# Performance work log

Hardware: AMD Instinct MI355X
Metric: run time of the kernel (lower is better)

The kernel has to match this reference:

```python
import jax, jax.numpy as jnp
import numpy as np

N_NODES = 50000
N_EDGES = 1600000
NODE_DIM = 64
EDGE_DIM = 64
HID = 64
EPS = 1e-5


def _linear(x, W, b):
    return x @ W + b


def _layernorm(x, g, b):
    m = jnp.mean(x, axis=-1, keepdims=True)
    v = jnp.mean((x - m) ** 2, axis=-1, keepdims=True)
    return (x - m) * jax.lax.rsqrt(v + EPS) * g + b


def _mlp(x, p, pre):
    # Linear-ReLU, Linear-ReLU, Linear-LayerNorm
    h = jax.nn.relu(_linear(x, p[pre + 'W1'], p[pre + 'b1']))
    h = jax.nn.relu(_linear(h, p[pre + 'W2'], p[pre + 'b2']))
    h = _linear(h, p[pre + 'W3'], p[pre + 'b3'])
    return _layernorm(h, p[pre + 'g'], p[pre + 'beta'])


def setup_inputs() -> dict:
    key = jax.random.key(0)
    ks = jax.random.split(key, 16)
    inp = {
        'node_feat': jax.random.normal(ks[0], (N_NODES, NODE_DIM), jnp.float32),
        'edge_feat': jax.random.normal(ks[1], (N_EDGES, EDGE_DIM), jnp.float32),
        'edge_idx': jax.random.randint(ks[2], (N_EDGES, 2), 0, N_NODES, jnp.int32),
        'node_size': N_NODES,
    }
    s = 0.05
    e_in = EDGE_DIM + 2 * NODE_DIM
    n_in = NODE_DIM + EDGE_DIM
    inp['eW1'] = jax.random.normal(ks[3], (e_in, HID), jnp.float32) * s
    inp['eb1'] = jnp.zeros((HID,), jnp.float32)
    inp['eW2'] = jax.random.normal(ks[4], (HID, HID), jnp.float32) * s
    inp['eb2'] = jnp.zeros((HID,), jnp.float32)
    inp['eW3'] = jax.random.normal(ks[5], (HID, HID), jnp.float32) * s
    inp['eb3'] = jnp.zeros((HID,), jnp.float32)
    inp['eg'] = jnp.ones((HID,), jnp.float32)
    inp['ebeta'] = jnp.zeros((HID,), jnp.float32)
    inp['nW1'] = jax.random.normal(ks[6], (n_in, HID), jnp.float32) * s
    inp['nb1'] = jnp.zeros((HID,), jnp.float32)
    inp['nW2'] = jax.random.normal(ks[7], (HID, HID), jnp.float32) * s
    inp['nb2'] = jnp.zeros((HID,), jnp.float32)
    inp['nW3'] = jax.random.normal(ks[8], (HID, HID), jnp.float32) * s
    inp['nb3'] = jnp.zeros((HID,), jnp.float32)
    inp['ng'] = jnp.ones((HID,), jnp.float32)
    inp['nbeta'] = jnp.zeros((HID,), jnp.float32)
    return inp


def reference(node_feat, edge_feat, edge_idx, node_size,
              eW1, eb1, eW2, eb2, eW3, eb3, eg, ebeta,
              nW1, nb1, nW2, nb2, nW3, nb3, ng, nbeta):
    p = dict(eW1=eW1, eb1=eb1, eW2=eW2, eb2=eb2, eW3=eW3, eb3=eb3, eg=eg, ebeta=ebeta,
             nW1=nW1, nb1=nb1, nW2=nW2, nb2=nb2, nW3=nW3, nb3=nb3, ng=ng, nbeta=nbeta)
    center = edge_idx[:, 0]
    source = edge_idx[:, 1]
    # [E, edge_dim + 2*node_dim]
    stacked = jnp.concatenate([edge_feat, node_feat[center], node_feat[source]], axis=1)
    proc_edge_feat = _mlp(stacked, p, 'e')  # [E, 64]
    # scatter-add aggregate to nodes
    nodal_edge_feat = jax.ops.segment_sum(proc_edge_feat, center, num_segments=node_size)
    stacked_node = jnp.concatenate([node_feat, nodal_edge_feat], axis=1)  # [N, node_dim+64]
    proc_node_feat = _mlp(stacked_node, p, 'n')  # [N, 64]
    return proc_edge_feat, proc_node_feat
```

## Files before the change

kernel.cpp:

```cpp
#include <hip/hip_runtime.h>

typedef unsigned short u16;
typedef unsigned int u32;
typedef __attribute__((ext_vector_type(8))) __bf16 bf16x8;
typedef __attribute__((ext_vector_type(4))) float f32x4;
typedef __attribute__((ext_vector_type(2))) u32 u32x2;
typedef __attribute__((ext_vector_type(4))) u32 u32x4;

__device__ __forceinline__ u16 f2bf(float f) {
    u32 u = __float_as_uint(f);
    u = (u + 0x7FFFu + ((u >> 16) & 1u)) >> 16;
    return (u16)u;
}
__device__ __forceinline__ bf16x8 cvt2bf(f32x4 lo, f32x4 hi) {
    bf16x8 r;
    r[0] = (__bf16)lo[0]; r[1] = (__bf16)lo[1]; r[2] = (__bf16)lo[2]; r[3] = (__bf16)lo[3];
    r[4] = (__bf16)hi[0]; r[5] = (__bf16)hi[1]; r[6] = (__bf16)hi[2]; r[7] = (__bf16)hi[3];
    return r;
}
__device__ __forceinline__ bf16x8 load8f_bf(const float* p) {
    return cvt2bf(*(const f32x4*)p, *(const f32x4*)(p + 4));
}
__device__ __forceinline__ u32 pk2(float x, float y) {
    __bf16 bx = (__bf16)x, by = (__bf16)y;
    return (u32)__builtin_bit_cast(u16, bx) | ((u32)__builtin_bit_cast(u16, by) << 16);
}

#define PK_EW1 0
#define PK_EW2 12288
#define PK_EW3 16384
#define PK_NW1 20480
#define PK_NW2 28672
#define PK_NW3 32768
#define PK_TOTAL 36864

__global__ void pack_weights_kernel(const float* __restrict__ eW1, const float* __restrict__ eW2,
                                    const float* __restrict__ eW3, const float* __restrict__ nW1,
                                    const float* __restrict__ nW2, const float* __restrict__ nW3,
                                    u16* __restrict__ P) {
    int idx = blockIdx.x * blockDim.x + threadIdx.x;
    if (idx >= PK_TOTAL) return;
    const float* W; int base;
    if (idx < PK_EW2)      { W = eW1; base = PK_EW1; }
    else if (idx < PK_EW3) { W = eW2; base = PK_EW2; }
    else if (idx < PK_NW1) { W = eW3; base = PK_EW3; }
    else if (idx < PK_NW2) { W = nW1; base = PK_NW1; }
    else if (idx < PK_NW3) { W = nW2; base = PK_NW2; }
    else                   { W = nW3; base = PK_NW3; }
    int r = idx - base;
    int j = r & 7, lane = (r >> 3) & 63, m = (r >> 9) & 3, s = r >> 11;
    int k = s * 32 + (lane >> 4) * 8 + j;
    int col = 16 * m + (lane & 15);
    P[idx] = f2bf(W[k * 64 + col]);
}

__global__ void degree_kernel(const int* __restrict__ edge_idx, int* __restrict__ deg, int E) {
    int e = blockIdx.x * blockDim.x + threadIdx.x;
    if (e < E) atomicAdd(&deg[edge_idx[2 * e]], 1);
}

__global__ void scan_blocks_kernel(const int* __restrict__ deg, int* __restrict__ off,
                                   int* __restrict__ partials, int N) {
    __shared__ int sh[256];
    const int t = threadIdx.x;
    const int g = blockIdx.x * 256 + t;
    int v = (g < N) ? deg[g] : 0;
    sh[t] = v;
    __syncthreads();
#pragma unroll
    for (int d = 1; d < 256; d <<= 1) {
        int add = (t >= d) ? sh[t - d] : 0;
        __syncthreads();
        sh[t] += add;
        __syncthreads();
    }
    if (g < N) off[g] = sh[t] - v;
    if (t == 255) partials[blockIdx.x] = sh[255];
}

__global__ void scan_partials_kernel(int* __restrict__ partials, int nparts) {
    __shared__ int sh[256];
    const int t = threadIdx.x;
    int v = (t < nparts) ? partials[t] : 0;
    sh[t] = v;
    __syncthreads();
#pragma unroll
    for (int d = 1; d < 256; d <<= 1) {
        int add = (t >= d) ? sh[t - d] : 0;
        __syncthreads();
        sh[t] += add;
        __syncthreads();
    }
    if (t < nparts) partials[t] = sh[t] - v;
}

__global__ void finalize_offsets_kernel(int* __restrict__ off, int* __restrict__ pos,
                                        const int* __restrict__ partials, int N, int E) {
    int g = blockIdx.x * blockDim.x + threadIdx.x;
    if (g < N) {
        int o = off[g] + partials[g >> 8];
        off[g] = o;
        pos[g] = o;
    }
    if (g == 0) off[N] = E;
}

__global__ void fill_csr_kernel(const int* __restrict__ edge_idx, int* __restrict__ pos,
                                int* __restrict__ csr, int E) {
    int e = blockIdx.x * blockDim.x + threadIdx.x;
    if (e < E) {
        int slot = atomicAdd(&pos[edge_idx[2 * e]], 1);
        csr[slot] = e;
    }
}

__global__ __launch_bounds__(256) void gather_kernel(
    const float* __restrict__ proc_edge, const int* __restrict__ off,
    const int* __restrict__ csr, u16* __restrict__ nodal16, int N)
{
    const int wid = threadIdx.x >> 6, lane = threadIdx.x & 63;
    const int n = blockIdx.x * 4 + wid;
    if (n >= N) return;
    const int r = lane >> 4;
    const int q = lane & 15;
    const int beg = off[n], end = off[n + 1];
    f32x4 v0 = 0.0f, v1 = 0.0f, v2 = 0.0f, v3 = 0.0f;
    int j = beg + r;
    for (; j + 12 < end; j += 16) {
        int e0 = csr[j], e1 = csr[j + 4], e2 = csr[j + 8], e3 = csr[j + 12];
        v0 += *(const f32x4*)(proc_edge + (size_t)e0 * 64 + q * 4);
        v1 += *(const f32x4*)(proc_edge + (size_t)e1 * 64 + q * 4);
        v2 += *(const f32x4*)(proc_edge + (size_t)e2 * 64 + q * 4);
        v3 += *(const f32x4*)(proc_edge + (size_t)e3 * 64 + q * 4);
    }
    for (; j < end; j += 4) {
        int e0 = csr[j];
        v0 += *(const f32x4*)(proc_edge + (size_t)e0 * 64 + q * 4);
    }
    v0 += v1; v2 += v3; v0 += v2;
#pragma unroll
    for (int i = 0; i < 4; ++i) {
        v0[i] += __shfl_xor(v0[i], 16, 64);
        v0[i] += __shfl_xor(v0[i], 32, 64);
    }
    if (r == 0) {
        u32x2 pv; pv[0] = pk2(v0[0], v0[1]); pv[1] = pk2(v0[2], v0[3]);
        *(u32x2*)(nodal16 + (size_t)n * 64 + q * 4) = pv;
    }
}

#define ET 2
__global__ __launch_bounds__(512, 6) void edge_mlp_kernel(
    const float* __restrict__ node_feat, const float* __restrict__ edge_feat,
    const int* __restrict__ edge_idx, const u16* __restrict__ Pw,
    const float* __restrict__ b1g, const float* __restrict__ b2g, const float* __restrict__ b3g,
    const float* __restrict__ gg, const float* __restrict__ betag,
    float* __restrict__ out_edge, int E)
{
    __shared__ u16 wlds[12288];
    __shared__ u16 htile[8][1024];
    __shared__ float params[5][64];
    const int tid = threadIdx.x;
#pragma unroll
    for (int i = 0; i < 3; ++i) {
        int idx = i * 512 + tid;
        *(u32x4*)(wlds + (size_t)idx * 8) = *(const u32x4*)(Pw + PK_EW1 + (size_t)idx * 8);
    }
    if (tid < 64) {
        params[0][tid] = b1g[tid];
        params[1][tid] = b2g[tid];
        params[2][tid] = b3g[tid];
        params[3][tid] = gg[tid];
        params[4][tid] = betag[tid];
    }
    __syncthreads();

    const int wid = tid >> 6, lane = tid & 63;
    const int er = lane & 15, a = lane >> 4;
    const int ebase = (blockIdx.x * 8 + wid) * (16 * ET);
    u16* ht = htile[wid];
    const int swz = (er & 7) << 4;

    int eidx[ET], cn[ET], sn[ET];
#pragma unroll
    for (int t = 0; t < ET; ++t) {
        int e = ebase + t * 16 + er;
        if (e > E - 1) e = E - 1;
        eidx[t] = e;
        int2 ii = *(const int2*)(edge_idx + 2 * e);
        cn[t] = ii.x; sn[t] = ii.y;
    }

    f32x4 acc[ET][4];
#pragma unroll
    for (int t = 0; t < ET; ++t)
#pragma unroll
        for (int m = 0; m < 4; ++m) acc[t][m] = 0.0f;

#pragma unroll
    for (int t = 0; t < ET; ++t) {
        f32x4 raw[12];
#pragma unroll
        for (int s = 0; s < 6; ++s) {
            const float* src;
            if (s < 2)      src = edge_feat + (size_t)eidx[t] * 64 + s * 32 + a * 8;
            else if (s < 4) src = node_feat + (size_t)cn[t] * 64 + (s - 2) * 32 + a * 8;
            else            src = node_feat + (size_t)sn[t] * 64 + (s - 4) * 32 + a * 8;
            raw[2 * s]     = *(const f32x4*)src;
            raw[2 * s + 1] = *(const f32x4*)(src + 4);
        }
#pragma unroll
        for (int s = 0; s < 6; ++s) {
            bf16x8 bf = cvt2bf(raw[2 * s], raw[2 * s + 1]);
#pragma unroll
            for (int m = 0; m < 4; ++m) {
                bf16x8 af = *(const bf16x8*)(wlds + ((s * 4 + m) * 64 + lane) * 8);
                acc[t][m] = __builtin_amdgcn_mfma_f32_16x16x32_bf16(af, bf, acc[t][m], 0, 0, 0);
            }
        }
    }
    __syncthreads();
#pragma unroll
    for (int i = 0; i < 2; ++i) {
        int idx = i * 512 + tid;
        *(u32x4*)(wlds + (size_t)idx * 8) = *(const u32x4*)(Pw + PK_EW2 + (size_t)idx * 8);
    }
    __syncthreads();

#pragma unroll
    for (int t = 0; t < ET; ++t) {
#pragma unroll
        for (int m = 0; m < 4; ++m) {
            float v0 = fmaxf(acc[t][m][0] + params[0][16 * m + 4 * a + 0], 0.0f);
            float v1 = fmaxf(acc[t][m][1] + params[0][16 * m + 4 * a + 1], 0.0f);
            float v2 = fmaxf(acc[t][m][2] + params[0][16 * m + 4 * a + 2], 0.0f);
            float v3 = fmaxf(acc[t][m][3] + params[0][16 * m + 4 * a + 3], 0.0f);
            u32x2 pv; pv[0] = pk2(v0, v1); pv[1] = pk2(v2, v3);
            int boff = (er * 128 + (16 * m + 4 * a) * 2) ^ swz;
            *(u32x2*)((char*)ht + boff) = pv;
        }
        f32x4 a2[4];
#pragma unroll
        for (int m = 0; m < 4; ++m) a2[m] = 0.0f;
#pragma unroll
        for (int s = 0; s < 2; ++s) {
            int boff = (er * 128 + s * 64 + a * 16) ^ swz;
            bf16x8 bf = *(const bf16x8*)((char*)ht + boff);
#pragma unroll
            for (int m = 0; m < 4; ++m) {
                bf16x8 af = *(const bf16x8*)(wlds + ((s * 4 + m) * 64 + lane) * 8);
                a2[m] = __builtin_amdgcn_mfma_f32_16x16x32_bf16(af, bf, a2[m], 0, 0, 0);
            }
        }
#pragma unroll
        for (int m = 0; m < 4; ++m) {
            float v0 = fmaxf(a2[m][0] + params[1][16 * m + 4 * a + 0], 0.0f);
            float v1 = fmaxf(a2[m][1] + params[1][16 * m + 4 * a + 1], 0.0f);
            float v2 = fmaxf(a2[m][2] + params[1][16 * m + 4 * a + 2], 0.0f);
            float v3 = fmaxf(a2[m][3] + params[1][16 * m + 4 * a + 3], 0.0f);
            u32x2 pv; pv[0] = pk2(v0, v1); pv[1] = pk2(v2, v3);
            int boff = (er * 128 + (16 * m + 4 * a) * 2) ^ swz;
            *(u32x2*)((char*)ht + boff) = pv;
        }
        f32x4 a3[4];
#pragma unroll
        for (int m = 0; m < 4; ++m) a3[m] = 0.0f;
#pragma unroll
        for (int s = 0; s < 2; ++s) {
            int boff = (er * 128 + s * 64 + a * 16) ^ swz;
            bf16x8 bf = *(const bf16x8*)((char*)ht + boff);
#pragma unroll
            for (int m = 0; m < 4; ++m) {
                bf16x8 af = *(const bf16x8*)(wlds + 4096 + ((s * 4 + m) * 64 + lane) * 8);
                a3[m] = __builtin_amdgcn_mfma_f32_16x16x32_bf16(af, bf, a3[m], 0, 0, 0);
            }
        }
        float vals[16], sum = 0.0f, ssq = 0.0f;
#pragma unroll
        for (int m = 0; m < 4; ++m)
#pragma unroll
            for (int r = 0; r < 4; ++r) {
                float v = a3[m][r] + params[2][16 * m + 4 * a + r];
                vals[4 * m + r] = v; sum += v; ssq += v * v;
            }
        sum += __shfl_xor(sum, 16, 64); sum += __shfl_xor(sum, 32, 64);
        ssq += __shfl_xor(ssq, 16, 64); ssq += __shfl_xor(ssq, 32, 64);
        const float mean = sum * 0.015625f;
        const float var = ssq * 0.015625f - mean * mean;
        const float inv = rsqrtf(var + 1e-5f);
        const int e = ebase + t * 16 + er;
        if (e < E) {
#pragma unroll
            for (int m = 0; m < 4; ++m) {
                f32x4 o;
#pragma unroll
                for (int r = 0; r < 4; ++r) {
                    int f = 16 * m + 4 * a + r;
                    o[r] = (vals[4 * m + r] - mean) * inv * params[3][f] + params[4][f];
                }
                *(f32x4*)(out_edge + (size_t)e * 64 + 16 * m + 4 * a) = o;
            }
        }
    }
}

__global__ __launch_bounds__(256) void node_mlp_kernel(
    const float* __restrict__ node_feat, const u16* __restrict__ nodal16,
    const u16* __restrict__ Pw,
    const float* __restrict__ b1g, const float* __restrict__ b2g, const float* __restrict__ b3g,
    const float* __restrict__ gg, const float* __restrict__ betag,
    float* __restrict__ out_node, int N)
{
    __shared__ float params[5][64];
    __shared__ u16 htile[4][1024];
    const int tid = threadIdx.x;
    if (tid < 64) {
        params[0][tid] = b1g[tid];
        params[1][tid] = b2g[tid];
        params[2][tid] = b3g[tid];
        params[3][tid] = gg[tid];
        params[4][tid] = betag[tid];
    }
    __syncthreads();
    const int wid = tid >> 6, lane = tid & 63;
    const int er = lane & 15, a = lane >> 4;
    const int nbase = (blockIdx.x * 4 + wid) * 16;
    if (nbase >= N) return;
    const int n = nbase + er;
    u16* ht = htile[wid];
    const int swz = (er & 7) << 4;

    f32x4 acc[4];
#pragma unroll
    for (int m = 0; m < 4; ++m) acc[m] = 0.0f;

#pragma unroll
    for (int s = 0; s < 4; ++s) {
        bf16x8 af[4];
#pragma unroll
        for (int m = 0; m < 4; ++m)
            af[m] = *(const bf16x8*)(Pw + PK_NW1 + ((s * 4 + m) * 64 + lane) * 8);
        bf16x8 bf;
        if (s < 2) bf = load8f_bf(node_feat + (size_t)n * 64 + s * 32 + a * 8);
        else       bf = *(const bf16x8*)(nodal16 + (size_t)n * 64 + (s - 2) * 32 + a * 8);
#pragma unroll
        for (int m = 0; m < 4; ++m)
            acc[m] = __builtin_amdgcn_mfma_f32_16x16x32_bf16(af[m], bf, acc[m], 0, 0, 0);
    }
#pragma unroll
    for (int m = 0; m < 4; ++m) {
        float v0 = fmaxf(acc[m][0] + params[0][16 * m + 4 * a + 0], 0.0f);
        float v1 = fmaxf(acc[m][1] + params[0][16 * m + 4 * a + 1], 0.0f);
        float v2 = fmaxf(acc[m][2] + params[0][16 * m + 4 * a + 2], 0.0f);
        float v3 = fmaxf(acc[m][3] + params[0][16 * m + 4 * a + 3], 0.0f);
        u32x2 pv; pv[0] = pk2(v0, v1); pv[1] = pk2(v2, v3);
        int boff = (er * 128 + (16 * m + 4 * a) * 2) ^ swz;
        *(u32x2*)((char*)ht + boff) = pv;
    }

#pragma unroll
    for (int m = 0; m < 4; ++m) acc[m] = 0.0f;
#pragma unroll
    for (int s = 0; s < 2; ++s) {
        bf16x8 af[4];
#pragma unroll
        for (int m = 0; m < 4; ++m)
            af[m] = *(const bf16x8*)(Pw + PK_NW2 + ((s * 4 + m) * 64 + lane) * 8);
        int boff = (er * 128 + s * 64 + a * 16) ^ swz;
        bf16x8 bf = *(const bf16x8*)((char*)ht + boff);
#pragma unroll
        for (int m = 0; m < 4; ++m)
            acc[m] = __builtin_amdgcn_mfma_f32_16x16x32_bf16(af[m], bf, acc[m], 0, 0, 0);
    }
#pragma unroll
    for (int m = 0; m < 4; ++m) {
        float v0 = fmaxf(acc[m][0] + params[1][16 * m + 4 * a + 0], 0.0f);
        float v1 = fmaxf(acc[m][1] + params[1][16 * m + 4 * a + 1], 0.0f);
        float v2 = fmaxf(acc[m][2] + params[1][16 * m + 4 * a + 2], 0.0f);
        float v3 = fmaxf(acc[m][3] + params[1][16 * m + 4 * a + 3], 0.0f);
        u32x2 pv; pv[0] = pk2(v0, v1); pv[1] = pk2(v2, v3);
        int boff = (er * 128 + (16 * m + 4 * a) * 2) ^ swz;
        *(u32x2*)((char*)ht + boff) = pv;
    }

#pragma unroll
    for (int m = 0; m < 4; ++m) acc[m] = 0.0f;
#pragma unroll
    for (int s = 0; s < 2; ++s) {
        bf16x8 af[4];
#pragma unroll
        for (int m = 0; m < 4; ++m)
            af[m] = *(const bf16x8*)(Pw + PK_NW3 + ((s * 4 + m) * 64 + lane) * 8);
        int boff = (er * 128 + s * 64 + a * 16) ^ swz;
        bf16x8 bf = *(const bf16x8*)((char*)ht + boff);
#pragma unroll
        for (int m = 0; m < 4; ++m)
            acc[m] = __builtin_amdgcn_mfma_f32_16x16x32_bf16(af[m], bf, acc[m], 0, 0, 0);
    }
    float vals[16], sum = 0.0f, ssq = 0.0f;
#pragma unroll
    for (int m = 0; m < 4; ++m)
#pragma unroll
        for (int r = 0; r < 4; ++r) {
            float v = acc[m][r] + params[2][16 * m + 4 * a + r];
            vals[4 * m + r] = v; sum += v; ssq += v * v;
        }
    sum += __shfl_xor(sum, 16, 64); sum += __shfl_xor(sum, 32, 64);
    ssq += __shfl_xor(ssq, 16, 64); ssq += __shfl_xor(ssq, 32, 64);
    const float mean = sum * 0.015625f;
    const float var = ssq * 0.015625f - mean * mean;
    const float inv = rsqrtf(var + 1e-5f);
#pragma unroll
    for (int m = 0; m < 4; ++m) {
        f32x4 o;
#pragma unroll
        for (int r = 0; r < 4; ++r) {
            int f = 16 * m + 4 * a + r;
            o[r] = (vals[4 * m + r] - mean) * inv * params[3][f] + params[4][f];
        }
        *(f32x4*)(out_node + (size_t)n * 64 + 16 * m + 4 * a) = o;
    }
}

extern "C" void kernel_launch(void* const* d_in, const int* in_sizes, int n_in,
                              void* d_out, int out_size, void* d_ws, size_t ws_size,
                              hipStream_t stream) {
    const float* node_feat = (const float*)d_in[0];
    const float* edge_feat = (const float*)d_in[1];
    const int* edge_idx  = (const int*)d_in[2];
    const float* eW1 = (const float*)d_in[4];
    const float* eb1 = (const float*)d_in[5];
    const float* eW2 = (const float*)d_in[6];
    const float* eb2 = (const float*)d_in[7];
    const float* eW3 = (const float*)d_in[8];
    const float* eb3 = (const float*)d_in[9];
    const float* eg  = (const float*)d_in[10];
    const float* ebt = (const float*)d_in[11];
    const float* nW1 = (const float*)d_in[12];
    const float* nb1 = (const float*)d_in[13];
    const float* nW2 = (const float*)d_in[14];
    const float* nb2 = (const float*)d_in[15];
    const float* nW3 = (const float*)d_in[16];
    const float* nb3 = (const float*)d_in[17];
    const float* ng  = (const float*)d_in[18];
    const float* nbt = (const float*)d_in[19];

    const int N = in_sizes[0] / 64;
    const int E = in_sizes[1] / 64;
    const int nparts = (N + 255) / 256;

    char* w = (char*)d_ws;
    int* off      = (int*)w;                    w += (size_t)(N + 1) * 4;
    int* pos      = (int*)w;                    w += (size_t)N * 4;
    int* partials = (int*)w;                    w += 256 * 4;
    int* csr      = (int*)w;                    w += (size_t)E * 4;
    u16* Pw       = (u16*)w;                    w += (size_t)PK_TOTAL * 2;
    u16* nodal16  = (u16*)w;

    float* out_edge = (float*)d_out;
    float* out_node = out_edge + (size_t)E * 64;

    pack_weights_kernel<<<(PK_TOTAL + 255) / 256, 256, 0, stream>>>(eW1, eW2, eW3, nW1, nW2, nW3, Pw);

    const int eblocks = (E + 255) / 256;
    edge_mlp_kernel<<<eblocks, 512, 0, stream>>>(node_feat, edge_feat, edge_idx, Pw,
                                                 eb1, eb2, eb3, eg, ebt, out_edge, E);

    hipMemsetAsync(pos, 0, (size_t)N * 4, stream);
    degree_kernel<<<(E + 255) / 256, 256, 0, stream>>>(edge_idx, pos, E);
    scan_blocks_kernel<<<nparts, 256, 0, stream>>>(pos, off, partials, N);
    scan_partials_kernel<<<1, 256, 0, stream>>>(partials, nparts);
    finalize_offsets_kernel<<<(N + 255) / 256, 256, 0, stream>>>(off, pos, partials, N, E);
    fill_csr_kernel<<<(E + 255) / 256, 256, 0, stream>>>(edge_idx, pos, csr, E);

    gather_kernel<<<(N + 3) / 4, 256, 0, stream>>>(out_edge, off, csr, nodal16, N);

    const int nblocks = (N + 63) / 64;
    node_mlp_kernel<<<nblocks, 256, 0, stream>>>(node_feat, nodal16, Pw,
                                                 nb1, nb2, nb3, ng, nbt, out_node, N);
}
```

Before: 570.6 us.

## Fuse segment-sum into edge MLP via CSR-ordered edges and atomic adds

Builds the CSR ordering before the edge MLP and processes edges in center-sorted order, so each wave's 16-edge tile shares center nodes. After layernorm, each wave writes its outputs to LDS, reduces runs of equal center indices, and atomically adds the partial sums into an fp32 nodal buffer. This removes the separate gather kernel and its re-read of the full edge output. In exchange, the edge kernel now gathers edge_feat and node_feat in scattered order, writes out_edge with scattered stores, uses fp32 atomics, and sums bf16-rounded values rather than fp32.

```diff
diff --git a/kernel.cpp b/kernel.cpp
--- a/kernel.cpp
+++ b/kernel.cpp
@@ -11,6 +11,9 @@
     u32 u = __float_as_uint(f);
     u = (u + 0x7FFFu + ((u >> 16) & 1u)) >> 16;
     return (u16)u;
+}
+__device__ __forceinline__ float bf2f(u16 h) {
+    return __uint_as_float(((u32)h) << 16);
 }
 __device__ __forceinline__ bf16x8 cvt2bf(f32x4 lo, f32x4 hi) {
     bf16x8 r;
@@ -114,51 +117,18 @@
     }
 }
 
-__global__ __launch_bounds__(256) void gather_kernel(
-    const float* __restrict__ proc_edge, const int* __restrict__ off,
-    const int* __restrict__ csr, u16* __restrict__ nodal16, int N)
-{
-    const int wid = threadIdx.x >> 6, lane = threadIdx.x & 63;
-    const int n = blockIdx.x * 4 + wid;
-    if (n >= N) return;
-    const int r = lane >> 4;
-    const int q = lane & 15;
-    const int beg = off[n], end = off[n + 1];
-    f32x4 v0 = 0.0f, v1 = 0.0f, v2 = 0.0f, v3 = 0.0f;
-    int j = beg + r;
-    for (; j + 12 < end; j += 16) {
-        int e0 = csr[j], e1 = csr[j + 4], e2 = csr[j + 8], e3 = csr[j + 12];
-        v0 += *(const f32x4*)(proc_edge + (size_t)e0 * 64 + q * 4);
-        v1 += *(const f32x4*)(proc_edge + (size_t)e1 * 64 + q * 4);
-        v2 += *(const f32x4*)(proc_edge + (size_t)e2 * 64 + q * 4);
-        v3 += *(const f32x4*)(proc_edge + (size_t)e3 * 64 + q * 4);
-    }
-    for (; j < end; j += 4) {
-        int e0 = csr[j];
-        v0 += *(const f32x4*)(proc_edge + (size_t)e0 * 64 + q * 4);
-    }
-    v0 += v1; v2 += v3; v0 += v2;
-#pragma unroll
-    for (int i = 0; i < 4; ++i) {
-        v0[i] += __shfl_xor(v0[i], 16, 64);
-        v0[i] += __shfl_xor(v0[i], 32, 64);
-    }
-    if (r == 0) {
-        u32x2 pv; pv[0] = pk2(v0[0], v0[1]); pv[1] = pk2(v0[2], v0[3]);
-        *(u32x2*)(nodal16 + (size_t)n * 64 + q * 4) = pv;
-    }
-}
-
 #define ET 2
 __global__ __launch_bounds__(512, 6) void edge_mlp_kernel(
     const float* __restrict__ node_feat, const float* __restrict__ edge_feat,
-    const int* __restrict__ edge_idx, const u16* __restrict__ Pw,
+    const int* __restrict__ edge_idx, const int* __restrict__ csr,
+    const u16* __restrict__ Pw,
     const float* __restrict__ b1g, const float* __restrict__ b2g, const float* __restrict__ b3g,
     const float* __restrict__ gg, const float* __restrict__ betag,
-    float* __restrict__ out_edge, int E)
+    float* __restrict__ out_edge, float* __restrict__ nodal, int E)
 {
     __shared__ u16 wlds[12288];
     __shared__ u16 htile[8][1024];
+    __shared__ int cnt[8][16];
     __shared__ float params[5][64];
     const int tid = threadIdx.x;
 #pragma unroll
@@ -177,15 +147,16 @@
 
     const int wid = tid >> 6, lane = tid & 63;
     const int er = lane & 15, a = lane >> 4;
-    const int ebase = (blockIdx.x * 8 + wid) * (16 * ET);
+    const int sbase = (blockIdx.x * 8 + wid) * (16 * ET);
     u16* ht = htile[wid];
     const int swz = (er & 7) << 4;
 
     int eidx[ET], cn[ET], sn[ET];
 #pragma unroll
     for (int t = 0; t < ET; ++t) {
-        int e = ebase + t * 16 + er;
-        if (e > E - 1) e = E - 1;
+        int slot = sbase + t * 16 + er;
+        if (slot > E - 1) slot = E - 1;
+        int e = csr[slot];
         eidx[t] = e;
         int2 ii = *(const int2*)(edge_idx + 2 * e);
         cn[t] = ii.x; sn[t] = ii.y;
@@ -288,24 +259,44 @@
         const float mean = sum * 0.015625f;
         const float var = ssq * 0.015625f - mean * mean;
         const float inv = rsqrtf(var + 1e-5f);
-        const int e = ebase + t * 16 + er;
-        if (e < E) {
-#pragma unroll
-            for (int m = 0; m < 4; ++m) {
-                f32x4 o;
-#pragma unroll
-                for (int r = 0; r < 4; ++r) {
-                    int f = 16 * m + 4 * a + r;
-                    o[r] = (vals[4 * m + r] - mean) * inv * params[3][f] + params[4][f];
+        const int slot = sbase + t * 16 + er;
+        const int e = eidx[t];
+#pragma unroll
+        for (int m = 0; m < 4; ++m) {
+            f32x4 o;
+#pragma unroll
+            for (int r = 0; r < 4; ++r) {
+                int f = 16 * m + 4 * a + r;
+                o[r] = (vals[4 * m + r] - mean) * inv * params[3][f] + params[4][f];
+            }
+            if (slot < E)
+                *(f32x4*)(out_edge + (size_t)e * 64 + 16 * m + 4 * a) = o;
+            u32x2 pv; pv[0] = pk2(o[0], o[1]); pv[1] = pk2(o[2], o[3]);
+            int boff = (er * 128 + (16 * m + 4 * a) * 2) ^ swz;
+            *(u32x2*)((char*)ht + boff) = pv;
+        }
+        if (a == 0) cnt[wid][er] = (slot < E) ? cn[t] : -1;
+        {
+            const int f = lane;
+            float accv = 0.0f;
+            int cprev = cnt[wid][0];
+#pragma unroll
+            for (int er2 = 0; er2 < 16; ++er2) {
+                int c = cnt[wid][er2];
+                if (c != cprev) {
+                    if (cprev >= 0) unsafeAtomicAdd(nodal + (size_t)cprev * 64 + f, accv);
+                    accv = 0.0f; cprev = c;
                 }
-                *(f32x4*)(out_edge + (size_t)e * 64 + 16 * m + 4 * a) = o;
-            }
+                int boff = (er2 * 128 + f * 2) ^ ((er2 & 7) << 4);
+                accv += bf2f(*(const u16*)((char*)ht + boff));
+            }
+            if (cprev >= 0) unsafeAtomicAdd(nodal + (size_t)cprev * 64 + f, accv);
         }
     }
 }
 
 __global__ __launch_bounds__(256) void node_mlp_kernel(
-    const float* __restrict__ node_feat, const u16* __restrict__ nodal16,
+    const float* __restrict__ node_feat, const float* __restrict__ nodal,
     const u16* __restrict__ Pw,
     const float* __restrict__ b1g, const float* __restrict__ b2g, const float* __restrict__ b3g,
     const float* __restrict__ gg, const float* __restrict__ betag,
@@ -342,7 +333,7 @@
             af[m] = *(const bf16x8*)(Pw + PK_NW1 + ((s * 4 + m) * 64 + lane) * 8);
         bf16x8 bf;
         if (s < 2) bf = load8f_bf(node_feat + (size_t)n * 64 + s * 32 + a * 8);
-        else       bf = *(const bf16x8*)(nodal16 + (size_t)n * 64 + (s - 2) * 32 + a * 8);
+        else       bf = load8f_bf(nodal + (size_t)n * 64 + (s - 2) * 32 + a * 8);
 #pragma unroll
         for (int m = 0; m < 4; ++m)
             acc[m] = __builtin_amdgcn_mfma_f32_16x16x32_bf16(af[m], bf, acc[m], 0, 0, 0);
@@ -455,27 +446,27 @@
     int* partials = (int*)w;                    w += 256 * 4;
     int* csr      = (int*)w;                    w += (size_t)E * 4;
     u16* Pw       = (u16*)w;                    w += (size_t)PK_TOTAL * 2;
-    u16* nodal16  = (u16*)w;
+    w = (char*)(((size_t)w + 255) & ~(size_t)255);
+    float* nodal  = (float*)w;
 
     float* out_edge = (float*)d_out;
     float* out_node = out_edge + (size_t)E * 64;
 
     pack_weights_kernel<<<(PK_TOTAL + 255) / 256, 256, 0, stream>>>(eW1, eW2, eW3, nW1, nW2, nW3, Pw);
 
-    const int eblocks = (E + 255) / 256;
-    edge_mlp_kernel<<<eblocks, 512, 0, stream>>>(node_feat, edge_feat, edge_idx, Pw,
-                                                 eb1, eb2, eb3, eg, ebt, out_edge, E);
-
     hipMemsetAsync(pos, 0, (size_t)N * 4, stream);
+    hipMemsetAsync(nodal, 0, (size_t)N * 64 * 4, stream);
     degree_kernel<<<(E + 255) / 256, 256, 0, stream>>>(edge_idx, pos, E);
     scan_blocks_kernel<<<nparts, 256, 0, stream>>>(pos, off, partials, N);
     scan_partials_kernel<<<1, 256, 0, stream>>>(partials, nparts);
     finalize_offsets_kernel<<<(N + 255) / 256, 256, 0, stream>>>(off, pos, partials, N, E);
     fill_csr_kernel<<<(E + 255) / 256, 256, 0, stream>>>(edge_idx, pos, csr, E);
 
-    gather_kernel<<<(N + 3) / 4, 256, 0, stream>>>(out_edge, off, csr, nodal16, N);
+    const int eblocks = (E + 255) / 256;
+    edge_mlp_kernel<<<eblocks, 512, 0, stream>>>(node_feat, edge_feat, edge_idx, csr, Pw,
+                                                 eb1, eb2, eb3, eg, ebt, out_edge, nodal, E);
 
     const int nblocks = (N + 63) / 64;
-    node_mlp_kernel<<<nblocks, 256, 0, stream>>>(node_feat, nodal16, Pw,
+    node_mlp_kernel<<<nblocks, 256, 0, stream>>>(node_feat, nodal, Pw,
                                                  nb1, nb2, nb3, ng, nbt, out_node, N);
 }
```

New measurement: 558.7 us. 2.1% less time.

## Scatter edge outputs as bf16 into CSR-sorted buffer for contiguous segment gather

Applied to the files above, without the earlier changes.

The CSR build now runs before the edge MLP and records each edge's slot (rank). The edge MLP writes a bf16 copy of its output at that slot, so the node aggregation reads contiguous rows instead of random fp32 rows through the csr index. The edge kernel also keeps all three edge weight matrices resident in LDS, which removes the mid-kernel reload and its syncs, and it issues all raw loads before the MFMAs. In exchange it adds an extra 128 B per edge of scattered writes, lowers the occupancy hint from 6 to 4 blocks, and needs a large workspace, falling back to the old gather if the workspace is too small.

```diff
diff --git a/kernel.cpp b/kernel.cpp
--- a/kernel.cpp
+++ b/kernel.cpp
@@ -33,6 +33,7 @@
 #define PK_NW2 28672
 #define PK_NW3 32768
 #define PK_TOTAL 36864
+#define EW_U16 20480
 
 __global__ void pack_weights_kernel(const float* __restrict__ eW1, const float* __restrict__ eW2,
                                     const float* __restrict__ eW3, const float* __restrict__ nW1,
@@ -106,15 +107,56 @@
 }
 
 __global__ void fill_csr_kernel(const int* __restrict__ edge_idx, int* __restrict__ pos,
-                                int* __restrict__ csr, int E) {
+                                int* __restrict__ csr, int* __restrict__ rank, int E) {
     int e = blockIdx.x * blockDim.x + threadIdx.x;
     if (e < E) {
         int slot = atomicAdd(&pos[edge_idx[2 * e]], 1);
         csr[slot] = e;
-    }
-}
-
-__global__ __launch_bounds__(256) void gather_kernel(
+        rank[e] = slot;
+    }
+}
+
+__global__ __launch_bounds__(256) void gather_sorted_kernel(
+    const u16* __restrict__ sorted16, const int* __restrict__ off,
+    u16* __restrict__ nodal16, int N)
+{
+    const int wid = threadIdx.x >> 6, lane = threadIdx.x & 63;
+    const int n = blockIdx.x * 4 + wid;
+    if (n >= N) return;
+    const int g = lane >> 3;
+    const int c = lane & 7;
+    const int beg = off[n], end = off[n + 1];
+    float va[8], vb[8];
+#pragma unroll
+    for (int i = 0; i < 8; ++i) { va[i] = 0.0f; vb[i] = 0.0f; }
+    int j = beg + g;
+    for (; j + 8 < end; j += 16) {
+        bf16x8 v1 = *(const bf16x8*)(sorted16 + (size_t)j * 64 + c * 8);
+        bf16x8 v2 = *(const bf16x8*)(sorted16 + (size_t)(j + 8) * 64 + c * 8);
+#pragma unroll
+        for (int i = 0; i < 8; ++i) { va[i] += (float)v1[i]; vb[i] += (float)v2[i]; }
+    }
+    if (j < end) {
+        bf16x8 v1 = *(const bf16x8*)(sorted16 + (size_t)j * 64 + c * 8);
+#pragma unroll
+        for (int i = 0; i < 8; ++i) va[i] += (float)v1[i];
+    }
+#pragma unroll
+    for (int i = 0; i < 8; ++i) {
+        va[i] += vb[i];
+        va[i] += __shfl_xor(va[i], 8, 64);
+        va[i] += __shfl_xor(va[i], 16, 64);
+        va[i] += __shfl_xor(va[i], 32, 64);
+    }
+    if (g == 0) {
+        u32x4 q;
+        q[0] = pk2(va[0], va[1]); q[1] = pk2(va[2], va[3]);
+        q[2] = pk2(va[4], va[5]); q[3] = pk2(va[6], va[7]);
+        *(u32x4*)(nodal16 + (size_t)n * 64 + c * 8) = q;
+    }
+}
+
+__global__ __launch_bounds__(256) void gather_csr_kernel(
     const float* __restrict__ proc_edge, const int* __restrict__ off,
     const int* __restrict__ csr, u16* __restrict__ nodal16, int N)
 {
@@ -150,21 +192,22 @@
 }
 
 #define ET 2
-__global__ __launch_bounds__(512, 6) void edge_mlp_kernel(
+__global__ __launch_bounds__(512, 4) void edge_mlp_kernel(
     const float* __restrict__ node_feat, const float* __restrict__ edge_feat,
-    const int* __restrict__ edge_idx, const u16* __restrict__ Pw,
+    const int* __restrict__ edge_idx, const int* __restrict__ rank,
+    const u16* __restrict__ Pw,
     const float* __restrict__ b1g, const float* __restrict__ b2g, const float* __restrict__ b3g,
     const float* __restrict__ gg, const float* __restrict__ betag,
-    float* __restrict__ out_edge, int E)
+    float* __restrict__ out_edge, u16* __restrict__ sorted16, int E)
 {
-    __shared__ u16 wlds[12288];
+    __shared__ u16 wlds[EW_U16];
     __shared__ u16 htile[8][1024];
     __shared__ float params[5][64];
     const int tid = threadIdx.x;
 #pragma unroll
-    for (int i = 0; i < 3; ++i) {
+    for (int i = 0; i < 5; ++i) {
         int idx = i * 512 + tid;
-        *(u32x4*)(wlds + (size_t)idx * 8) = *(const u32x4*)(Pw + PK_EW1 + (size_t)idx * 8);
+        *(u32x4*)(wlds + (size_t)idx * 8) = *(const u32x4*)(Pw + (size_t)idx * 8);
     }
     if (tid < 64) {
         params[0][tid] = b1g[tid];
@@ -181,7 +224,7 @@
     u16* ht = htile[wid];
     const int swz = (er & 7) << 4;
 
-    int eidx[ET], cn[ET], sn[ET];
+    int eidx[ET], cn[ET], sn[ET], rk[ET];
 #pragma unroll
     for (int t = 0; t < ET; ++t) {
         int e = ebase + t * 16 + er;
@@ -189,43 +232,38 @@
         eidx[t] = e;
         int2 ii = *(const int2*)(edge_idx + 2 * e);
         cn[t] = ii.x; sn[t] = ii.y;
-    }
-
-    f32x4 acc[ET][4];
+        rk[t] = sorted16 ? rank[e] : 0;
+    }
+
+    f32x4 raw[ET][12];
 #pragma unroll
     for (int t = 0; t < ET; ++t)
-#pragma unroll
-        for (int m = 0; m < 4; ++m) acc[t][m] = 0.0f;
-
-#pragma unroll
-    for (int t = 0; t < ET; ++t) {
-        f32x4 raw[12];
 #pragma unroll
         for (int s = 0; s < 6; ++s) {
             const float* src;
             if (s < 2)      src = edge_feat + (size_t)eidx[t] * 64 + s * 32 + a * 8;
             else if (s < 4) src = node_feat + (size_t)cn[t] * 64 + (s - 2) * 32 + a * 8;
             else            src = node_feat + (size_t)sn[t] * 64 + (s - 4) * 32 + a * 8;
-            raw[2 * s]     = *(const f32x4*)src;
-            raw[2 * s + 1] = *(const f32x4*)(src + 4);
-        }
+            raw[t][2 * s]     = *(const f32x4*)src;
+            raw[t][2 * s + 1] = *(const f32x4*)(src + 4);
+        }
+
+    f32x4 acc[ET][4];
+#pragma unroll
+    for (int t = 0; t < ET; ++t)
+#pragma unroll
+        for (int m = 0; m < 4; ++m) acc[t][m] = 0.0f;
+#pragma unroll
+    for (int t = 0; t < ET; ++t)
 #pragma unroll
         for (int s = 0; s < 6; ++s) {
-            bf16x8 bf = cvt2bf(raw[2 * s], raw[2 * s + 1]);
+            bf16x8 bf = cvt2bf(raw[t][2 * s], raw[t][2 * s + 1]);
 #pragma unroll
             for (int m = 0; m < 4; ++m) {
-                bf16x8 af = *(const bf16x8*)(wlds + ((s * 4 + m) * 64 + lane) * 8);
+                bf16x8 af = *(const bf16x8*)(wlds + PK_EW1 + ((s * 4 + m) * 64 + lane) * 8);
                 acc[t][m] = __builtin_amdgcn_mfma_f32_16x16x32_bf16(af, bf, acc[t][m], 0, 0, 0);
             }
         }
-    }
-    __syncthreads();
-#pragma unroll
-    for (int i = 0; i < 2; ++i) {
-        int idx = i * 512 + tid;
-        *(u32x4*)(wlds + (size_t)idx * 8) = *(const u32x4*)(Pw + PK_EW2 + (size_t)idx * 8);
-    }
-    __syncthreads();
 
 #pragma unroll
     for (int t = 0; t < ET; ++t) {
@@ -248,7 +286,7 @@
             bf16x8 bf = *(const bf16x8*)((char*)ht + boff);
 #pragma unroll
             for (int m = 0; m < 4; ++m) {
-                bf16x8 af = *(const bf16x8*)(wlds + ((s * 4 + m) * 64 + lane) * 8);
+                bf16x8 af = *(const bf16x8*)(wlds + PK_EW2 + ((s * 4 + m) * 64 + lane) * 8);
                 a2[m] = __builtin_amdgcn_mfma_f32_16x16x32_bf16(af, bf, a2[m], 0, 0, 0);
             }
         }
@@ -271,7 +309,7 @@
             bf16x8 bf = *(const bf16x8*)((char*)ht + boff);
 #pragma unroll
             for (int m = 0; m < 4; ++m) {
-                bf16x8 af = *(const bf16x8*)(wlds + 4096 + ((s * 4 + m) * 64 + lane) * 8);
+                bf16x8 af = *(const bf16x8*)(wlds + PK_EW3 + ((s * 4 + m) * 64 + lane) * 8);
                 a3[m] = __builtin_amdgcn_mfma_f32_16x16x32_bf16(af, bf, a3[m], 0, 0, 0);
             }
         }
@@ -289,16 +327,20 @@
         const float var = ssq * 0.015625f - mean * mean;
         const float inv = rsqrtf(var + 1e-5f);
         const int e = ebase + t * 16 + er;
-        if (e < E) {
-#pragma unroll
-            for (int m = 0; m < 4; ++m) {
-                f32x4 o;
-#pragma unroll
-                for (int r = 0; r < 4; ++r) {
-                    int f = 16 * m + 4 * a + r;
-                    o[r] = (vals[4 * m + r] - mean) * inv * params[3][f] + params[4][f];
+#pragma unroll
+        for (int m = 0; m < 4; ++m) {
+            f32x4 o;
+#pragma unroll
+            for (int r = 0; r < 4; ++r) {
+                int f = 16 * m + 4 * a + r;
+                o[r] = (vals[4 * m + r] - mean) * inv * params[3][f] + params[4][f];
+            }
+            if (e < E) {
+                *(f32x4*)(out_edge + (size_t)e * 64 + 16 * m + 4 * a) = o;
+                if (sorted16) {
+                    u32x2 pv; pv[0] = pk2(o[0], o[1]); pv[1] = pk2(o[2], o[3]);
+                    *(u32x2*)(sorted16 + (size_t)rk[t] * 64 + 16 * m + 4 * a) = pv;
                 }
-                *(f32x4*)(out_edge + (size_t)e * 64 + 16 * m + 4 * a) = o;
             }
         }
     }
@@ -449,31 +491,41 @@
     const int E = in_sizes[1] / 64;
     const int nparts = (N + 255) / 256;
 
-    char* w = (char*)d_ws;
+    char* w0 = (char*)d_ws;
+    char* w = w0;
     int* off      = (int*)w;                    w += (size_t)(N + 1) * 4;
     int* pos      = (int*)w;                    w += (size_t)N * 4;
     int* partials = (int*)w;                    w += 256 * 4;
     int* csr      = (int*)w;                    w += (size_t)E * 4;
+    int* rank     = (int*)w;                    w += (size_t)E * 4;
     u16* Pw       = (u16*)w;                    w += (size_t)PK_TOTAL * 2;
-    u16* nodal16  = (u16*)w;
+    w = (char*)(((size_t)w + 255) & ~(size_t)255);
+    u16* nodal16  = (u16*)w;                    w += (size_t)N * 64 * 2;
+    w = (char*)(((size_t)w + 255) & ~(size_t)255);
+    u16* sorted16 = (u16*)w;                    w += (size_t)E * 64 * 2;
+    const bool use_sorted = ((size_t)(w - w0) <= ws_size);
 
     float* out_edge = (float*)d_out;
     float* out_node = out_edge + (size_t)E * 64;
 
     pack_weights_kernel<<<(PK_TOTAL + 255) / 256, 256, 0, stream>>>(eW1, eW2, eW3, nW1, nW2, nW3, Pw);
-
-    const int eblocks = (E + 255) / 256;
-    edge_mlp_kernel<<<eblocks, 512, 0, stream>>>(node_feat, edge_feat, edge_idx, Pw,
-                                                 eb1, eb2, eb3, eg, ebt, out_edge, E);
 
     hipMemsetAsync(pos, 0, (size_t)N * 4, stream);
     degree_kernel<<<(E + 255) / 256, 256, 0, stream>>>(edge_idx, pos, E);
     scan_blocks_kernel<<<nparts, 256, 0, stream>>>(pos, off, partials, N);
     scan_partials_kernel<<<1, 256, 0, stream>>>(partials, nparts);
     finalize_offsets_kernel<<<(N + 255) / 256, 256, 0, stream>>>(off, pos, partials, N, E);
-    fill_csr_kernel<<<(E + 255) / 256, 256, 0, stream>>>(edge_idx, pos, csr, E);
-
-    gather_kernel<<<(N + 3) / 4, 256, 0, stream>>>(out_edge, off, csr, nodal16, N);
+    fill_csr_kernel<<<(E + 255) / 256, 256, 0, stream>>>(edge_idx, pos, csr, rank, E);
+
+    const int eblocks = (E + 255) / 256;
+    edge_mlp_kernel<<<eblocks, 512, 0, stream>>>(node_feat, edge_feat, edge_idx, rank, Pw,
+                                                 eb1, eb2, eb3, eg, ebt, out_edge,
+                                                 use_sorted ? sorted16 : (u16*)nullptr, E);
+
+    if (use_sorted)
+        gather_sorted_kernel<<<(N + 3) / 4, 256, 0, stream>>>(sorted16, off, nodal16, N);
+    else
+        gather_csr_kernel<<<(N + 3) / 4, 256, 0, stream>>>(out_edge, off, csr, nodal16, N);
 
     const int nblocks = (N + 63) / 64;
     node_mlp_kernel<<<nblocks, 256, 0, stream>>>(node_feat, nodal16, Pw,
```

Result: slower. 642.2 us (+12.5%).

## Stage edge MLP input gathers through direct global-to-LDS loads

Applied to the files above, without the earlier changes.

The edge MLP kernel now loads the edge and node feature rows with global_load_lds straight into a per-wave LDS staging buffer, waits on vmcnt, then reads them back from LDS for the bf16 conversion and MFMA. It also changes from two 16-edge tiles per wave with 512-thread blocks to one tile per wave with 256-thread blocks. The intent is to cut register pressure and raise occupancy while keeping the gather loads asynchronous. The cost is a larger LDS footprint per block, an extra LDS round trip, and less work in flight per wave.

```diff
diff --git a/kernel.cpp b/kernel.cpp
--- a/kernel.cpp
+++ b/kernel.cpp
@@ -114,7 +114,7 @@
     }
 }
 
-__global__ __launch_bounds__(256) void gather_kernel(
+__global__ __launch_bounds__(256) void gather_csr_kernel(
     const float* __restrict__ proc_edge, const int* __restrict__ off,
     const int* __restrict__ csr, u16* __restrict__ nodal16, int N)
 {
@@ -149,8 +149,7 @@
     }
 }
 
-#define ET 2
-__global__ __launch_bounds__(512, 6) void edge_mlp_kernel(
+__global__ __launch_bounds__(256) void edge_mlp_kernel(
     const float* __restrict__ node_feat, const float* __restrict__ edge_feat,
     const int* __restrict__ edge_idx, const u16* __restrict__ Pw,
     const float* __restrict__ b1g, const float* __restrict__ b2g, const float* __restrict__ b3g,
@@ -158,12 +157,12 @@
     float* __restrict__ out_edge, int E)
 {
     __shared__ u16 wlds[12288];
-    __shared__ u16 htile[8][1024];
+    __shared__ u16 stage[4][6144];
     __shared__ float params[5][64];
     const int tid = threadIdx.x;
 #pragma unroll
-    for (int i = 0; i < 3; ++i) {
-        int idx = i * 512 + tid;
+    for (int i = 0; i < 6; ++i) {
+        int idx = i * 256 + tid;
         *(u32x4*)(wlds + (size_t)idx * 8) = *(const u32x4*)(Pw + PK_EW1 + (size_t)idx * 8);
     }
     if (tid < 64) {
@@ -177,129 +176,122 @@
 
     const int wid = tid >> 6, lane = tid & 63;
     const int er = lane & 15, a = lane >> 4;
-    const int ebase = (blockIdx.x * 8 + wid) * (16 * ET);
-    u16* ht = htile[wid];
+    const int e0 = blockIdx.x * 64 + wid * 16 + er;
+    const int e = (e0 < E) ? e0 : (E - 1);
+    int2 ii = *(const int2*)(edge_idx + 2 * e);
+    const int cn = ii.x, sn = ii.y;
+    u16* st = stage[wid];
     const int swz = (er & 7) << 4;
 
-    int eidx[ET], cn[ET], sn[ET];
-#pragma unroll
-    for (int t = 0; t < ET; ++t) {
-        int e = ebase + t * 16 + er;
-        if (e > E - 1) e = E - 1;
-        eidx[t] = e;
-        int2 ii = *(const int2*)(edge_idx + 2 * e);
-        cn[t] = ii.x; sn[t] = ii.y;
-    }
-
-    f32x4 acc[ET][4];
-#pragma unroll
-    for (int t = 0; t < ET; ++t)
-#pragma unroll
-        for (int m = 0; m < 4; ++m) acc[t][m] = 0.0f;
-
-#pragma unroll
-    for (int t = 0; t < ET; ++t) {
-        f32x4 raw[12];
-#pragma unroll
-        for (int s = 0; s < 6; ++s) {
-            const float* src;
-            if (s < 2)      src = edge_feat + (size_t)eidx[t] * 64 + s * 32 + a * 8;
-            else if (s < 4) src = node_feat + (size_t)cn[t] * 64 + (s - 2) * 32 + a * 8;
-            else            src = node_feat + (size_t)sn[t] * 64 + (s - 4) * 32 + a * 8;
-            raw[2 * s]     = *(const f32x4*)src;
-            raw[2 * s + 1] = *(const f32x4*)(src + 4);
-        }
-#pragma unroll
-        for (int s = 0; s < 6; ++s) {
-            bf16x8 bf = cvt2bf(raw[2 * s], raw[2 * s + 1]);
-#pragma unroll
-            for (int m = 0; m < 4; ++m) {
-                bf16x8 af = *(const bf16x8*)(wlds + ((s * 4 + m) * 64 + lane) * 8);
-                acc[t][m] = __builtin_amdgcn_mfma_f32_16x16x32_bf16(af, bf, acc[t][m], 0, 0, 0);
+#pragma unroll
+    for (int s = 0; s < 6; ++s) {
+        const float* base;
+        if (s < 2)      base = edge_feat + (size_t)e * 64 + s * 32 + a * 8;
+        else if (s < 4) base = node_feat + (size_t)cn * 64 + (s - 2) * 32 + a * 8;
+        else            base = node_feat + (size_t)sn * 64 + (s - 4) * 32 + a * 8;
+        __builtin_amdgcn_global_load_lds(
+            (const __attribute__((address_space(1))) void*)base,
+            (__attribute__((address_space(3))) void*)(st + (2 * s) * 512), 16, 0, 0);
+        __builtin_amdgcn_global_load_lds(
+            (const __attribute__((address_space(1))) void*)(base + 4),
+            (__attribute__((address_space(3))) void*)(st + (2 * s + 1) * 512), 16, 0, 0);
+    }
+    __builtin_amdgcn_sched_barrier(0);
+    asm volatile("s_waitcnt vmcnt(0)" ::: "memory");
+    __builtin_amdgcn_sched_barrier(0);
+
+    f32x4 acc[4];
+#pragma unroll
+    for (int m = 0; m < 4; ++m) acc[m] = 0.0f;
+#pragma unroll
+    for (int s = 0; s < 6; ++s) {
+        f32x4 lo = *(const f32x4*)((const char*)st + (2 * s) * 1024 + lane * 16);
+        f32x4 hi = *(const f32x4*)((const char*)st + (2 * s + 1) * 1024 + lane * 16);
+        bf16x8 bf = cvt2bf(lo, hi);
+#pragma unroll
+        for (int m = 0; m < 4; ++m) {
+            bf16x8 af = *(const bf16x8*)(wlds + ((s * 4 + m) * 64 + lane) * 8);
+            acc[m] = __builtin_amdgcn_mfma_f32_16x16x32_bf16(af, bf, acc[m], 0, 0, 0);
+        }
+    }
+    __syncthreads();
+#pragma unroll
+    for (int i = 0; i < 4; ++i) {
+        int idx = i * 256 + tid;
+        *(u32x4*)(wlds + (size_t)idx * 8) = *(const u32x4*)(Pw + PK_EW2 + (size_t)idx * 8);
+    }
+    __syncthreads();
+
+    u16* ht = st;
+#pragma unroll
+    for (int m = 0; m < 4; ++m) {
+        float v0 = fmaxf(acc[m][0] + params[0][16 * m + 4 * a + 0], 0.0f);
+        float v1 = fmaxf(acc[m][1] + params[0][16 * m + 4 * a + 1], 0.0f);
+        float v2 = fmaxf(acc[m][2] + params[0][16 * m + 4 * a + 2], 0.0f);
+        float v3 = fmaxf(acc[m][3] + params[0][16 * m + 4 * a + 3], 0.0f);
+        u32x2 pv; pv[0] = pk2(v0, v1); pv[1] = pk2(v2, v3);
+        int boff = (er * 128 + (16 * m + 4 * a) * 2) ^ swz;
+        *(u32x2*)((char*)ht + boff) = pv;
+    }
+    f32x4 a2[4];
+#pragma unroll
+    for (int m = 0; m < 4; ++m) a2[m] = 0.0f;
+#pragma unroll
+    for (int s = 0; s < 2; ++s) {
+        int boff = (er * 128 + s * 64 + a * 16) ^ swz;
+        bf16x8 bf = *(const bf16x8*)((char*)ht + boff);
+#pragma unroll
+        for (int m = 0; m < 4; ++m) {
+            bf16x8 af = *(const bf16x8*)(wlds + ((s * 4 + m) * 64 + lane) * 8);
+            a2[m] = __builtin_amdgcn_mfma_f32_16x16x32_bf16(af, bf, a2[m], 0, 0, 0);
+        }
+    }
+#pragma unroll
+    for (int m = 0; m < 4; ++m) {
+        float v0 = fmaxf(a2[m][0] + params[1][16 * m + 4 * a + 0], 0.0f);
+        float v1 = fmaxf(a2[m][1] + params[1][16 * m + 4 * a + 1], 0.0f);
+        float v2 = fmaxf(a2[m][2] + params[1][16 * m + 4 * a + 2], 0.0f);
+        float v3 = fmaxf(a2[m][3] + params[1][16 * m + 4 * a + 3], 0.0f);
+        u32x2 pv; pv[0] = pk2(v0, v1); pv[1] = pk2(v2, v3);
+        int boff = (er * 128 + (16 * m + 4 * a) * 2) ^ swz;
+        *(u32x2*)((char*)ht + boff) = pv;
+    }
+    f32x4 a3[4];
+#pragma unroll
+    for (int m = 0; m < 4; ++m) a3[m] = 0.0f;
+#pragma unroll
+    for (int s = 0; s < 2; ++s) {
+        int boff = (er * 128 + s * 64 + a * 16) ^ swz;
+        bf16x8 bf = *(const bf16x8*)((char*)ht + boff);
+#pragma unroll
+        for (int m = 0; m < 4; ++m) {
+            bf16x8 af = *(const bf16x8*)(wlds + 4096 + ((s * 4 + m) * 64 + lane) * 8);
+            a3[m] = __builtin_amdgcn_mfma_f32_16x16x32_bf16(af, bf, a3[m], 0, 0, 0);
+        }
+    }
+    float vals[16], sum = 0.0f, ssq = 0.0f;
+#pragma unroll
+    for (int m = 0; m < 4; ++m)
+#pragma unroll
+        for (int r = 0; r < 4; ++r) {
+            float v = a3[m][r] + params[2][16 * m + 4 * a + r];
+            vals[4 * m + r] = v; sum += v; ssq += v * v;
+        }
+    sum += __shfl_xor(sum, 16, 64); sum += __shfl_xor(sum, 32, 64);
+    ssq += __shfl_xor(ssq, 16, 64); ssq += __shfl_xor(ssq, 32, 64);
+    const float mean = sum * 0.015625f;
+    const float var = ssq * 0.015625f - mean * mean;
+    const float inv = rsqrtf(var + 1e-5f);
+    if (e0 < E) {
+#pragma unroll
+        for (int m = 0; m < 4; ++m) {
+            f32x4 o;
+#pragma unroll
+            for (int r = 0; r < 4; ++r) {
+                int f = 16 * m + 4 * a + r;
+                o[r] = (vals[4 * m + r] - mean) * inv * params[3][f] + params[4][f];
             }
-        }
-    }
-    __syncthreads();
-#pragma unroll
-    for (int i = 0; i < 2; ++i) {
-        int idx = i * 512 + tid;
-        *(u32x4*)(wlds + (size_t)idx * 8) = *(const u32x4*)(Pw + PK_EW2 + (size_t)idx * 8);
-    }
-    __syncthreads();
-
-#pragma unroll
-    for (int t = 0; t < ET; ++t) {
-#pragma unroll
-        for (int m = 0; m < 4; ++m) {
-            float v0 = fmaxf(acc[t][m][0] + params[0][16 * m + 4 * a + 0], 0.0f);
-            float v1 = fmaxf(acc[t][m][1] + params[0][16 * m + 4 * a + 1], 0.0f);
-            float v2 = fmaxf(acc[t][m][2] + params[0][16 * m + 4 * a + 2], 0.0f);
-            float v3 = fmaxf(acc[t][m][3] + params[0][16 * m + 4 * a + 3], 0.0f);
-            u32x2 pv; pv[0] = pk2(v0, v1); pv[1] = pk2(v2, v3);
-            int boff = (er * 128 + (16 * m + 4 * a) * 2) ^ swz;
-            *(u32x2*)((char*)ht + boff) = pv;
-        }
-        f32x4 a2[4];
-#pragma unroll
-        for (int m = 0; m < 4; ++m) a2[m] = 0.0f;
-#pragma unroll
-        for (int s = 0; s < 2; ++s) {
-            int boff = (er * 128 + s * 64 + a * 16) ^ swz;
-            bf16x8 bf = *(const bf16x8*)((char*)ht + boff);
-#pragma unroll
-            for (int m = 0; m < 4; ++m) {
-                bf16x8 af = *(const bf16x8*)(wlds + ((s * 4 + m) * 64 + lane) * 8);
-                a2[m] = __builtin_amdgcn_mfma_f32_16x16x32_bf16(af, bf, a2[m], 0, 0, 0);
-            }
-        }
-#pragma unroll
-        for (int m = 0; m < 4; ++m) {
-            float v0 = fmaxf(a2[m][0] + params[1][16 * m + 4 * a + 0], 0.0f);
-            float v1 = fmaxf(a2[m][1] + params[1][16 * m + 4 * a + 1], 0.0f);
-            float v2 = fmaxf(a2[m][2] + params[1][16 * m + 4 * a + 2], 0.0f);
-            float v3 = fmaxf(a2[m][3] + params[1][16 * m + 4 * a + 3], 0.0f);
-            u32x2 pv; pv[0] = pk2(v0, v1); pv[1] = pk2(v2, v3);
-            int boff = (er * 128 + (16 * m + 4 * a) * 2) ^ swz;
-            *(u32x2*)((char*)ht + boff) = pv;
-        }
-        f32x4 a3[4];
-#pragma unroll
-        for (int m = 0; m < 4; ++m) a3[m] = 0.0f;
-#pragma unroll
-        for (int s = 0; s < 2; ++s) {
-            int boff = (er * 128 + s * 64 + a * 16) ^ swz;
-            bf16x8 bf = *(const bf16x8*)((char*)ht + boff);
-#pragma unroll
-            for (int m = 0; m < 4; ++m) {
-                bf16x8 af = *(const bf16x8*)(wlds + 4096 + ((s * 4 + m) * 64 + lane) * 8);
-                a3[m] = __builtin_amdgcn_mfma_f32_16x16x32_bf16(af, bf, a3[m], 0, 0, 0);
-            }
-        }
-        float vals[16], sum = 0.0f, ssq = 0.0f;
-#pragma unroll
-        for (int m = 0; m < 4; ++m)
-#pragma unroll
-            for (int r = 0; r < 4; ++r) {
-                float v = a3[m][r] + params[2][16 * m + 4 * a + r];
-                vals[4 * m + r] = v; sum += v; ssq += v * v;
-            }
-        sum += __shfl_xor(sum, 16, 64); sum += __shfl_xor(sum, 32, 64);
-        ssq += __shfl_xor(ssq, 16, 64); ssq += __shfl_xor(ssq, 32, 64);
-        const float mean = sum * 0.015625f;
-        const float var = ssq * 0.015625f - mean * mean;
-        const float inv = rsqrtf(var + 1e-5f);
-        const int e = ebase + t * 16 + er;
-        if (e < E) {
-#pragma unroll
-            for (int m = 0; m < 4; ++m) {
-                f32x4 o;
-#pragma unroll
-                for (int r = 0; r < 4; ++r) {
-                    int f = 16 * m + 4 * a + r;
-                    o[r] = (vals[4 * m + r] - mean) * inv * params[3][f] + params[4][f];
-                }
-                *(f32x4*)(out_edge + (size_t)e * 64 + 16 * m + 4 * a) = o;
-            }
+            *(f32x4*)(out_edge + (size_t)e0 * 64 + 16 * m + 4 * a) = o;
         }
     }
 }
@@ -455,6 +447,7 @@
     int* partials = (int*)w;                    w += 256 * 4;
     int* csr      = (int*)w;                    w += (size_t)E * 4;
     u16* Pw       = (u16*)w;                    w += (size_t)PK_TOTAL * 2;
+    w = (char*)(((size_t)w + 255) & ~(size_t)255);
     u16* nodal16  = (u16*)w;
 
     float* out_edge = (float*)d_out;
@@ -462,8 +455,8 @@
 
     pack_weights_kernel<<<(PK_TOTAL + 255) / 256, 256, 0, stream>>>(eW1, eW2, eW3, nW1, nW2, nW3, Pw);
 
-    const int eblocks = (E + 255) / 256;
-    edge_mlp_kernel<<<eblocks, 512, 0, stream>>>(node_feat, edge_feat, edge_idx, Pw,
+    const int eblocks = (E + 63) / 64;
+    edge_mlp_kernel<<<eblocks, 256, 0, stream>>>(node_feat, edge_feat, edge_idx, Pw,
                                                  eb1, eb2, eb3, eg, ebt, out_edge, E);
 
     hipMemsetAsync(pos, 0, (size_t)N * 4, stream);
@@ -473,7 +466,7 @@
     finalize_offsets_kernel<<<(N + 255) / 256, 256, 0, stream>>>(off, pos, partials, N, E);
     fill_csr_kernel<<<(E + 255) / 256, 256, 0, stream>>>(edge_idx, pos, csr, E);
 
-    gather_kernel<<<(N + 3) / 4, 256, 0, stream>>>(out_edge, off, csr, nodal16, N);
+    gather_csr_kernel<<<(N + 3) / 4, 256, 0, stream>>>(out_edge, off, csr, nodal16, N);
 
     const int nblocks = (N + 63) / 64;
     node_mlp_kernel<<<nblocks, 256, 0, stream>>>(node_feat, nodal16, Pw,
```

New measurement: 654.6 us. +14.7%, slower.
